# Optimization experiments

Hardware: AMD Instinct MI355X
Metric: run time of the kernel (lower is better)

The kernel has to match this reference:

```python
import jax, jax.numpy as jnp
import numpy as np

NUM_HEADS = 4   # forced by reshape(B, N, num_heads, C) of a dim*4 projection
BN_EPS = 1e-5


def _chamfer(a, b):
    # a, b: [B, N, 3] -> symmetric chamfer distance (mean of nearest sq-dists)
    d = (jnp.sum(a ** 2, -1)[:, :, None] + jnp.sum(b ** 2, -1)[:, None, :]
         - 2.0 * jnp.einsum('bnc,bmc->bnm', a, b))
    return jnp.mean(jnp.min(d, axis=2)) + jnp.mean(jnp.min(d, axis=1))


def _forward(xs, pc1, bn_gamma, bn_beta, q_w, kv_w, proj_w, proj_b, map_w, map_b):
    B, F, C, N = xs.shape
    H = NUM_HEADS
    scale = C ** -0.5  # head_dim == dim in this module (full-dim heads)

    def per_item(x):  # x: [F, C, N]
        # BatchNorm1d in eval mode (running_mean=0, running_var=1)
        xn = (x / jnp.sqrt(1.0 + BN_EPS)) * bn_gamma[:, None] + bn_beta[:, None]
        xn = xn.transpose(0, 2, 1)                 # [F, N, C]
        xr = xn[::-1]                              # flip over frame axis
        q = (xn @ q_w.T).reshape(F, N, H, C).transpose(0, 2, 1, 3)        # [F,H,N,C]
        kv = (xr @ kv_w.T).reshape(F, N, 2, H, C).transpose(2, 0, 3, 1, 4)
        k, v = kv[0], kv[1]                        # [F,H,N,C]
        attn = jax.nn.softmax(jnp.einsum('fhnc,fhmc->fhnm', q, k) * scale, axis=-1)
        o = jnp.einsum('fhnm,fhmc->fhnc', attn, v).transpose(0, 2, 1, 3)  # [F,N,H,C]
        xa = (o[0] + o[1]).transpose(1, 0, 2)      # [H, N, C]: sum of first two frames
        xa = xa @ proj_w.T + proj_b                # [H, N, C] x_appearance
        fr = xa @ map_w.T + map_b                  # [H, N, 3] frames (mapping_xyz)
        return xa, fr

    xa, frames = jax.vmap(per_item)(xs)            # [B,H,N,C], [B,H,N,3]
    pc1t = pc1.transpose(0, 2, 1)                  # [B, N, 3]
    loss = _chamfer(pc1t + frames[:, 0], pc1t)
    return xa[:, 1:], frames[:, 1:], loss


def setup_inputs() -> dict:
    key = jax.random.key(0)
    ks = jax.random.split(key, 8)
    B, F, C, N = 2, 4, 64, 2048
    return {
        'xs': jax.random.normal(ks[0], (B, F, C, N), jnp.float32),
        'pc1': jax.random.normal(ks[1], (B, 3, N), jnp.float32),
        'pc2': jax.random.normal(ks[2], (B, 3, N), jnp.float32),
        'bn_gamma': jnp.ones((C,), jnp.float32),
        'bn_beta': jnp.zeros((C,), jnp.float32),
        'q_w': 0.02 * jax.random.normal(ks[3], (4 * C, C), jnp.float32),
        'kv_w': 0.02 * jax.random.normal(ks[4], (8 * C, C), jnp.float32),
        'proj_w': 0.02 * jax.random.normal(ks[5], (C, C), jnp.float32),
        'proj_b': jnp.zeros((C,), jnp.float32),
        'map_w': 0.02 * jax.random.normal(ks[6], (3, C), jnp.float32),
        'map_b': jnp.zeros((3,), jnp.float32),
    }


def reference(xs, pc1, pc2, bn_gamma, bn_beta, q_w, kv_w, proj_w, proj_b, map_w, map_b):
    # pc2 is accepted by the torch forward but unused in its body
    return _forward(xs, pc1, bn_gamma, bn_beta, q_w, kv_w, proj_w, proj_b, map_w, map_b)
```

## Files before the change

kernel.cpp:

```cpp
#include <hip/hip_runtime.h>
#include <hip/hip_bf16.h>

#define NPTS 2048
#define LOG2E 1.4426950408889634f
#define NJC 16
#define JCH 128

typedef short bf16x8 __attribute__((ext_vector_type(8)));
typedef float f32x4 __attribute__((ext_vector_type(4)));
typedef unsigned uint32x4 __attribute__((ext_vector_type(4)));
typedef __attribute__((address_space(3))) char lds_char;
typedef __attribute__((address_space(1))) const char glob_char;

union PBU { uint32x4 u; bf16x8 v; };

static __device__ __forceinline__ unsigned cvt_pk_bf16(float a, float b) {
    unsigned r;
    asm("v_cvt_pk_bf16_f32 %0, %1, %2" : "=v"(r) : "v"(a), "v"(b));
    return r;
}
static __device__ __forceinline__ float b2f(unsigned short u) {
    return __uint_as_float((unsigned)u << 16);
}

__global__ void prep_weights(const float* __restrict__ gamma, const float* __restrict__ beta,
                             const float* __restrict__ q_w, const float* __restrict__ kv_w,
                             float* __restrict__ Wp, float* __restrict__ bp) {
    int j = blockIdx.x * blockDim.x + threadIdx.x;
    if (j >= 768) return;
    const float inv = 1.0f / sqrtf(1.0f + 1e-5f);
    const float* src;
    float scale;
    if (j < 256) { src = q_w + j * 64;          scale = 0.125f * LOG2E; }
    else         { src = kv_w + (j - 256) * 64; scale = 1.0f; }
    float b = 0.f;
    for (int c = 0; c < 64; ++c) {
        float w = src[c];
        Wp[j * 64 + c] = w * gamma[c] * inv * scale;
        b += w * beta[c];
    }
    bp[j] = b * scale;
}

__global__ __launch_bounds__(256) void qkv_gemm(const float* __restrict__ xs,
                                                const float* __restrict__ Wp,
                                                const float* __restrict__ bp,
                                                __hip_bfloat16* __restrict__ Qg,
                                                __hip_bfloat16* __restrict__ Kg,
                                                __hip_bfloat16* __restrict__ Vtg) {
    const int bf = blockIdx.z;
    const int b = bf >> 1, f01 = bf & 1;
    const int jt = blockIdx.y;
    const int f_src = (jt < 4) ? f01 : (3 - f01);
    const int n0 = blockIdx.x * 64;
    const float* __restrict__ A = xs + (size_t)((b * 4 + f_src) * 64) * NPTS;

    __shared__ float As[64][68];
    __shared__ float Ws[64][68];

    const int t = threadIdx.x;
    const int tx = t & 15, ty = t >> 4;

    for (int r = 0; r < 4; ++r) {
        int row = ty + 16 * r;
        int col = tx * 4;
        *(float4*)&As[row][col] = *(const float4*)&A[(size_t)row * NPTS + n0 + col];
        *(float4*)&Ws[row][col] = *(const float4*)&Wp[(size_t)(jt * 64 + row) * 64 + col];
    }
    __syncthreads();

    float acc[4][4];
#pragma unroll
    for (int jj = 0; jj < 4; ++jj) {
        float bv = bp[jt * 64 + tx + 16 * jj];
#pragma unroll
        for (int i = 0; i < 4; ++i) acc[i][jj] = bv;
    }
    for (int c = 0; c < 64; ++c) {
        float a[4], w[4];
#pragma unroll
        for (int i = 0; i < 4; ++i) a[i] = As[c][ty + 16 * i];
#pragma unroll
        for (int jj = 0; jj < 4; ++jj) w[jj] = Ws[tx + 16 * jj][c];
#pragma unroll
        for (int i = 0; i < 4; ++i)
#pragma unroll
            for (int jj = 0; jj < 4; ++jj) acc[i][jj] += a[i] * w[jj];
    }

    if (jt < 8) {
        __hip_bfloat16* __restrict__ dst = (jt < 4 ? Qg : Kg) + (size_t)bf * NPTS * 256;
        const int jb = (jt & 3) * 64;
#pragma unroll
        for (int i = 0; i < 4; ++i) {
            int n = n0 + ty + 16 * i;
#pragma unroll
            for (int jj = 0; jj < 4; ++jj)
                dst[(size_t)n * 256 + jb + tx + 16 * jj] = __float2bfloat16(acc[i][jj]);
        }
    } else {
        __syncthreads();
#pragma unroll
        for (int i = 0; i < 4; ++i)
#pragma unroll
            for (int jj = 0; jj < 4; ++jj)
                As[tx + 16 * jj][ty + 16 * i] = acc[i][jj];
        __syncthreads();
        const int row = t >> 2, c0 = (t & 3) * 16;
        __hip_bfloat16* __restrict__ dst =
            Vtg + ((size_t)bf * 256 + (jt - 8) * 64 + row) * NPTS + n0 + c0;
#pragma unroll
        for (int c = 0; c < 16; ++c) dst[c] = __float2bfloat16(As[row][c0 + c]);
    }
}

__global__ __launch_bounds__(256, 4) void attn_mfma(const __hip_bfloat16* __restrict__ Qg,
                                                    const __hip_bfloat16* __restrict__ Kg,
                                                    const __hip_bfloat16* __restrict__ Vtg,
                                                    __hip_bfloat16* __restrict__ OTb,
                                                    float* __restrict__ Lp) {
    const int combo = blockIdx.x;
    const int bf = combo >> 2, h = combo & 3;
    const int n0 = blockIdx.y * 128;
    const int split = blockIdx.z;
    const int kbase = split * (NPTS / 4);
    const int NT = NPTS / 4 / 64;

    __shared__ __align__(16) char smem[32768];

    const int t = threadIdx.x;
    const int lane = t & 63, w = t >> 6;
    const int l15 = lane & 15, g = lane >> 4;
    const int srow = lane >> 3, sslot = lane & 7;

    const __hip_bfloat16* qbase =
        Qg + ((size_t)bf * NPTS + n0 + w * 32 + l15) * 256 + h * 64 + g * 8;
    bf16x8 qf[2][2];
    qf[0][0] = *(const bf16x8*)(qbase);
    qf[0][1] = *(const bf16x8*)(qbase + 32);
    qf[1][0] = *(const bf16x8*)(qbase + 16 * 256);
    qf[1][1] = *(const bf16x8*)(qbase + 16 * 256 + 32);

    const __hip_bfloat16* kgb = Kg + (size_t)bf * NPTS * 256 + h * 64;
    const __hip_bfloat16* vgb = Vtg + ((size_t)bf * 256 + h * 64) * NPTS;

    int ldsoff[4][2];
#pragma unroll
    for (int tt = 0; tt < 4; ++tt) {
        const int row = tt * 16 + l15;
#pragma unroll
        for (int s = 0; s < 2; ++s)
            ldsoff[tt][s] = row * 128 + (((s * 4 + g) ^ (row & 7)) << 4);
    }

    f32x4 oacc[2][4];
    float lsum0 = 0.f, lsum1 = 0.f;
#pragma unroll
    for (int f = 0; f < 2; ++f)
#pragma unroll
        for (int r = 0; r < 4; ++r) oacc[f][r] = (f32x4){0.f, 0.f, 0.f, 0.f};

    auto stage = [&](int kt, int bsel) {
#pragma unroll
        for (int ii = 0; ii < 2; ++ii) {
            const int rb = w * 16 + ii * 8;
            const int r = rb + srow;
            const int cs = (sslot ^ (r & 7)) * 8;
            const __hip_bfloat16* ksrc = kgb + (size_t)(kbase + kt * 64 + r) * 256 + cs;
            __builtin_amdgcn_global_load_lds((const glob_char*)ksrc,
                (lds_char*)(smem + bsel * 16384 + rb * 128), 16, 0, 0);
            const __hip_bfloat16* vsrc = vgb + (size_t)r * NPTS + kbase + kt * 64 + cs;
            __builtin_amdgcn_global_load_lds((const glob_char*)vsrc,
                (lds_char*)(smem + bsel * 16384 + 8192 + rb * 128), 16, 0, 0);
        }
    };

    stage(0, 0);
    int cur = 0;

    for (int kt = 0; kt < NT; ++kt) {
        if (kt < NT - 1) {
            stage(kt + 1, cur ^ 1);
            asm volatile("s_waitcnt vmcnt(4)" ::: "memory");
        } else {
            asm volatile("s_waitcnt vmcnt(0)" ::: "memory");
        }
        __builtin_amdgcn_s_barrier();
        asm volatile("" ::: "memory");

        const char* Kt = smem + cur * 16384;
        const char* Vt = Kt + 8192;

        bf16x8 kf[4][2];
#pragma unroll
        for (int tt = 0; tt < 4; ++tt) {
            kf[tt][0] = *(const bf16x8*)(Kt + ldsoff[tt][0]);
            kf[tt][1] = *(const bf16x8*)(Kt + ldsoff[tt][1]);
        }

        bf16x8 pb0[2], pb1[2];

        {
            f32x4 st[4];
            __builtin_amdgcn_s_setprio(1);
#pragma unroll
            for (int tt = 0; tt < 4; ++tt) {
                f32x4 z = (f32x4){0.f, 0.f, 0.f, 0.f};
                z = __builtin_amdgcn_mfma_f32_16x16x32_bf16(kf[tt][0], qf[0][0], z, 0, 0, 0);
                z = __builtin_amdgcn_mfma_f32_16x16x32_bf16(kf[tt][1], qf[0][1], z, 0, 0, 0);
                st[tt] = z;
            }
            __builtin_amdgcn_s_setprio(0);
            unsigned c0[4], c1[4];
#pragma unroll
            for (int tt = 0; tt < 4; ++tt) {
                float p0 = exp2f(fminf(st[tt][0], 126.f));
                float p1 = exp2f(fminf(st[tt][1], 126.f));
                float p2 = exp2f(fminf(st[tt][2], 126.f));
                float p3 = exp2f(fminf(st[tt][3], 126.f));
                lsum0 += (p0 + p1) + (p2 + p3);
                c0[tt] = cvt_pk_bf16(p0, p1);
                c1[tt] = cvt_pk_bf16(p2, p3);
            }
#pragma unroll
            for (int s = 0; s < 2; ++s) {
                unsigned x0 = c0[2 * s], y0 = c0[2 * s + 1];
                unsigned x1 = c1[2 * s], y1 = c1[2 * s + 1];
                asm("v_permlane32_swap_b32 %0, %1" : "+v"(x0), "+v"(y0));
                asm("v_permlane16_swap_b32 %0, %1" : "+v"(x0), "+v"(y0));
                asm("v_permlane32_swap_b32 %0, %1" : "+v"(x1), "+v"(y1));
                asm("v_permlane16_swap_b32 %0, %1" : "+v"(x1), "+v"(y1));
                PBU pu;
                pu.u = (uint32x4){x0, x1, y0, y1};
                pb0[s] = pu.v;
            }
        }

        {
            f32x4 st[4];
            __builtin_amdgcn_s_setprio(1);
#pragma unroll
            for (int tt = 0; tt < 4; ++tt) {
                f32x4 z = (f32x4){0.f, 0.f, 0.f, 0.f};
                z = __builtin_amdgcn_mfma_f32_16x16x32_bf16(kf[tt][0], qf[1][0], z, 0, 0, 0);
                z = __builtin_amdgcn_mfma_f32_16x16x32_bf16(kf[tt][1], qf[1][1], z, 0, 0, 0);
                st[tt] = z;
            }
            __builtin_amdgcn_s_setprio(0);
            unsigned c0[4], c1[4];
#pragma unroll
            for (int tt = 0; tt < 4; ++tt) {
                float p0 = exp2f(fminf(st[tt][0], 126.f));
                float p1 = exp2f(fminf(st[tt][1], 126.f));
                float p2 = exp2f(fminf(st[tt][2], 126.f));
                float p3 = exp2f(fminf(st[tt][3], 126.f));
                lsum1 += (p0 + p1) + (p2 + p3);
                c0[tt] = cvt_pk_bf16(p0, p1);
                c1[tt] = cvt_pk_bf16(p2, p3);
            }
#pragma unroll
            for (int s = 0; s < 2; ++s) {
                unsigned x0 = c0[2 * s], y0 = c0[2 * s + 1];
                unsigned x1 = c1[2 * s], y1 = c1[2 * s + 1];
                asm("v_permlane32_swap_b32 %0, %1" : "+v"(x0), "+v"(y0));
                asm("v_permlane16_swap_b32 %0, %1" : "+v"(x0), "+v"(y0));
                asm("v_permlane32_swap_b32 %0, %1" : "+v"(x1), "+v"(y1));
                asm("v_permlane16_swap_b32 %0, %1" : "+v"(x1), "+v"(y1));
                PBU pu;
                pu.u = (uint32x4){x0, x1, y0, y1};
                pb1[s] = pu.v;
            }
        }

        __builtin_amdgcn_s_setprio(1);
#pragma unroll
        for (int ct = 0; ct < 4; ++ct) {
            bf16x8 vf0 = *(const bf16x8*)(Vt + ldsoff[ct][0]);
            bf16x8 vf1 = *(const bf16x8*)(Vt + ldsoff[ct][1]);
            f32x4 z0 = oacc[0][ct];
            z0 = __builtin_amdgcn_mfma_f32_16x16x32_bf16(vf0, pb0[0], z0, 0, 0, 0);
            z0 = __builtin_amdgcn_mfma_f32_16x16x32_bf16(vf1, pb0[1], z0, 0, 0, 0);
            oacc[0][ct] = z0;
            f32x4 z1 = oacc[1][ct];
            z1 = __builtin_amdgcn_mfma_f32_16x16x32_bf16(vf0, pb1[0], z1, 0, 0, 0);
            z1 = __builtin_amdgcn_mfma_f32_16x16x32_bf16(vf1, pb1[1], z1, 0, 0, 0);
            oacc[1][ct] = z1;
        }
        __builtin_amdgcn_s_setprio(0);

        asm volatile("s_waitcnt lgkmcnt(0)" ::: "memory");
        __builtin_amdgcn_s_barrier();
        asm volatile("" ::: "memory");
        cur ^= 1;
    }

    lsum0 += __shfl_xor(lsum0, 16);
    lsum0 += __shfl_xor(lsum0, 32);
    lsum1 += __shfl_xor(lsum1, 16);
    lsum1 += __shfl_xor(lsum1, 32);
    const int qq = n0 + w * 32 + l15;
    if (g == 0) {
        Lp[(size_t)(split * 16 + combo) * NPTS + qq] = lsum0;
        Lp[(size_t)(split * 16 + combo) * NPTS + qq + 16] = lsum1;
    }

    __hip_bfloat16* __restrict__ Op = OTb + (size_t)(split * 16 + combo) * 64 * NPTS;
#pragma unroll
    for (int ct = 0; ct < 4; ++ct)
#pragma unroll
        for (int r = 0; r < 4; ++r) {
            Op[(size_t)(ct * 16 + g * 4 + r) * NPTS + qq] = __float2bfloat16(oacc[0][ct][r]);
            Op[(size_t)(ct * 16 + g * 4 + r) * NPTS + qq + 16] = __float2bfloat16(oacc[1][ct][r]);
        }
}

__global__ __launch_bounds__(256) void proj_frames(const __hip_bfloat16* __restrict__ OTb,
                                                   const float* __restrict__ Lp,
                                                   const float* __restrict__ proj_w,
                                                   const float* __restrict__ proj_b,
                                                   const float* __restrict__ map_w,
                                                   const float* __restrict__ map_b,
                                                   float* __restrict__ out,
                                                   float* __restrict__ frames0) {
    const int bh = blockIdx.y, b = bh >> 2, h = bh & 3;
    const int n0 = blockIdx.x * 64;
    const int cf0 = (b * 2 + 0) * 4 + h;
    const int cf1 = (b * 2 + 1) * 4 + h;

    __shared__ float Xs[64][68];
    __shared__ float Ws[64][68];
    __shared__ float xaS[64][68];

    const int t = threadIdx.x;
    const int tx = t & 15, ty = t >> 4;
    const int nc = n0 + tx * 4;

    float4 L0 = make_float4(0.f, 0.f, 0.f, 0.f), L1 = L0;
#pragma unroll
    for (int s = 0; s < 4; ++s) {
        float4 a = *(const float4*)&Lp[(size_t)(s * 16 + cf0) * NPTS + nc];
        L0.x += a.x; L0.y += a.y; L0.z += a.z; L0.w += a.w;
        float4 c = *(const float4*)&Lp[(size_t)(s * 16 + cf1) * NPTS + nc];
        L1.x += c.x; L1.y += c.y; L1.z += c.z; L1.w += c.w;
    }
    float4 inv0 = make_float4(1.f / L0.x, 1.f / L0.y, 1.f / L0.z, 1.f / L0.w);
    float4 inv1 = make_float4(1.f / L1.x, 1.f / L1.y, 1.f / L1.z, 1.f / L1.w);

    for (int r = 0; r < 4; ++r) {
        int row = ty + 16 * r, col = tx * 4;
        float x0 = 0.f, x1 = 0.f, x2 = 0.f, x3 = 0.f;
        float y0 = 0.f, y1 = 0.f, y2 = 0.f, y3 = 0.f;
#pragma unroll
        for (int s = 0; s < 4; ++s) {
            ushort4 u0 = *(const ushort4*)&OTb[((size_t)(s * 16 + cf0) * 64 + row) * NPTS + n0 + col];
            ushort4 u1 = *(const ushort4*)&OTb[((size_t)(s * 16 + cf1) * 64 + row) * NPTS + n0 + col];
            x0 += b2f(u0.x); x1 += b2f(u0.y); x2 += b2f(u0.z); x3 += b2f(u0.w);
            y0 += b2f(u1.x); y1 += b2f(u1.y); y2 += b2f(u1.z); y3 += b2f(u1.w);
        }
        Xs[row][col + 0] = x0 * inv0.x + y0 * inv1.x;
        Xs[row][col + 1] = x1 * inv0.y + y1 * inv1.y;
        Xs[row][col + 2] = x2 * inv0.z + y2 * inv1.z;
        Xs[row][col + 3] = x3 * inv0.w + y3 * inv1.w;
        *(float4*)&Ws[row][col] = *(const float4*)&proj_w[(size_t)row * 64 + col];
    }
    __syncthreads();

    float acc[4][4];
#pragma unroll
    for (int jj = 0; jj < 4; ++jj) {
        float bv = proj_b[tx + 16 * jj];
#pragma unroll
        for (int i = 0; i < 4; ++i) acc[i][jj] = bv;
    }
    for (int c = 0; c < 64; ++c) {
        float a[4], w[4];
#pragma unroll
        for (int i = 0; i < 4; ++i) a[i] = Xs[c][ty + 16 * i];
#pragma unroll
        for (int jj = 0; jj < 4; ++jj) w[jj] = Ws[tx + 16 * jj][c];
#pragma unroll
        for (int i = 0; i < 4; ++i)
#pragma unroll
            for (int jj = 0; jj < 4; ++jj) acc[i][jj] += a[i] * w[jj];
    }

#pragma unroll
    for (int i = 0; i < 4; ++i)
#pragma unroll
        for (int jj = 0; jj < 4; ++jj)
            xaS[ty + 16 * i][tx + 16 * jj] = acc[i][jj];

    if (h >= 1) {
        float* __restrict__ xa_out = out + (size_t)(b * 3 + h - 1) * NPTS * 64;
#pragma unroll
        for (int i = 0; i < 4; ++i)
#pragma unroll
            for (int jj = 0; jj < 4; ++jj)
                xa_out[(size_t)(n0 + ty + 16 * i) * 64 + tx + 16 * jj] = acc[i][jj];
    }
    __syncthreads();

    if (t < 192) {
        int r = t / 3, j = t % 3;
        float s = map_b[j];
        for (int c = 0; c < 64; ++c) s += xaS[r][c] * map_w[j * 64 + c];
        int n = n0 + r;
        if (h == 0) frames0[((size_t)b * NPTS + n) * 3 + j] = s;
        else        out[786432 + ((size_t)(b * 3 + h - 1) * NPTS + n) * 3 + j] = s;
    }
}

__global__ __launch_bounds__(256) void chamfer_partial(const float* __restrict__ pc1,
                                                       const float* __restrict__ frames0,
                                                       float* __restrict__ partial) {
    const int z = blockIdx.z;
    const int dir = z >> 1, b = z & 1;
    const int i = blockIdx.x * 256 + threadIdx.x;
    const int j0 = blockIdx.y * JCH;
    const float* __restrict__ px = pc1 + (size_t)b * 3 * NPTS;
    const float* __restrict__ fr = frames0 + (size_t)b * NPTS * 3;

    __shared__ float4 sj[JCH];
    if (threadIdx.x < JCH) {
        int jj = j0 + threadIdx.x;
        float bx = px[jj], by = px[NPTS + jj], bz = px[2 * NPTS + jj];
        if (dir == 1) { bx += fr[jj * 3]; by += fr[jj * 3 + 1]; bz += fr[jj * 3 + 2]; }
        sj[threadIdx.x] = make_float4(bx, by, bz, bx * bx + by * by + bz * bz);
    }
    float ax = px[i], ay = px[NPTS + i], az = px[2 * NPTS + i];
    if (dir == 0) { ax += fr[i * 3]; ay += fr[i * 3 + 1]; az += fr[i * 3 + 2]; }
    const float a2 = ax * ax + ay * ay + az * az;
    __syncthreads();

    float best = 1e30f;
#pragma unroll 4
    for (int k = 0; k < JCH; ++k) {
        float4 p = sj[k];
        float d = a2 + p.w - 2.0f * (ax * p.x + ay * p.y + az * p.z);
        best = fminf(best, d);
    }
    partial[((size_t)z * NJC + blockIdx.y) * NPTS + i] = best;
}

__global__ __launch_bounds__(256) void chamfer_minsum(const float* __restrict__ partial,
                                                      double* __restrict__ sums) {
    const int gid = blockIdx.x * 256 + threadIdx.x;
    const int z = gid >> 11, i = gid & 2047;
    float best = 1e30f;
#pragma unroll
    for (int c = 0; c < NJC; ++c)
        best = fminf(best, partial[((size_t)z * NJC + c) * NPTS + i]);
    __shared__ double sm[256];
    sm[threadIdx.x] = (double)best;
    __syncthreads();
    for (int off = 128; off > 0; off >>= 1) {
        if (threadIdx.x < off) sm[threadIdx.x] += sm[threadIdx.x + off];
        __syncthreads();
    }
    if (threadIdx.x == 0) sums[blockIdx.x] = sm[0];
}

__global__ void chamfer_final(const double* __restrict__ sums, float* __restrict__ loss_out) {
    if (threadIdx.x == 0) {
        double s = 0.0;
        for (int k = 0; k < 32; ++k) s += sums[k];
        loss_out[0] = (float)(s / 4096.0);
    }
}

extern "C" void kernel_launch(void* const* d_in, const int* in_sizes, int n_in,
                              void* d_out, int out_size, void* d_ws, size_t ws_size,
                              hipStream_t stream) {
    const float* xs     = (const float*)d_in[0];
    const float* pc1    = (const float*)d_in[1];
    const float* gamma  = (const float*)d_in[3];
    const float* beta   = (const float*)d_in[4];
    const float* q_w    = (const float*)d_in[5];
    const float* kv_w   = (const float*)d_in[6];
    const float* proj_w = (const float*)d_in[7];
    const float* proj_b = (const float*)d_in[8];
    const float* map_w  = (const float*)d_in[9];
    const float* map_b  = (const float*)d_in[10];
    float* out = (float*)d_out;

    char* ws = (char*)d_ws;
    __hip_bfloat16* Qg  = (__hip_bfloat16*)(ws);
    __hip_bfloat16* Kg  = (__hip_bfloat16*)(ws + 4194304);
    __hip_bfloat16* Vtg = (__hip_bfloat16*)(ws + 8388608);
    __hip_bfloat16* OTb = (__hip_bfloat16*)(ws + 12582912);
    float* Wp      = (float*)(ws + 29360128);
    float* bp      = (float*)(ws + 29556736);
    float* frames0 = (float*)(ws + 29559808);
    float* partial = (float*)(ws + 29609984);
    double* sums   = (double*)(ws + 30134272);
    float* Lp      = (float*)(ws + 30134528);

    hipLaunchKernelGGL(prep_weights, dim3(3), dim3(256), 0, stream,
                       gamma, beta, q_w, kv_w, Wp, bp);
    hipLaunchKernelGGL(qkv_gemm, dim3(32, 12, 4), dim3(256), 0, stream,
                       xs, Wp, bp, Qg, Kg, Vtg);
    hipLaunchKernelGGL(attn_mfma, dim3(16, 16, 4), dim3(256), 0, stream,
                       Qg, Kg, Vtg, OTb, Lp);
    hipLaunchKernelGGL(proj_frames, dim3(32, 8), dim3(256), 0, stream,
                       OTb, Lp, proj_w, proj_b, map_w, map_b, out, frames0);
    hipLaunchKernelGGL(chamfer_partial, dim3(NPTS / 256, NJC, 4), dim3(256), 0, stream,
                       pc1, frames0, partial);
    hipLaunchKernelGGL(chamfer_minsum, dim3(32), dim3(256), 0, stream,
                       partial, sums);
    hipLaunchKernelGGL(chamfer_final, dim3(1), dim3(64), 0, stream,
                       sums, out + 823296);
}
```

Measured before the change: 91.86 us.

## Shrink attention KV tile to 32 rows with 4-slot ring buffer, two-deep prefetch

The attention kernel now processes 32-key tiles instead of 64 and cycles them through a 4-entry LDS ring with two tiles prefetched ahead. That allows one barrier per tile instead of two. The V LDS layout and swizzle change to match the narrower tile. The aim is better overlap of global-to-LDS loads with MFMA work and less barrier stall, at the cost of twice as many loop iterations and barriers per key range. The setprio hints are also dropped.

```diff
diff --git a/kernel.cpp b/kernel.cpp
--- a/kernel.cpp
+++ b/kernel.cpp
@@ -124,14 +124,18 @@
     const int n0 = blockIdx.y * 128;
     const int split = blockIdx.z;
     const int kbase = split * (NPTS / 4);
-    const int NT = NPTS / 4 / 64;
+    const int NT = NPTS / 4 / 32;
 
     __shared__ __align__(16) char smem[32768];
 
     const int t = threadIdx.x;
     const int lane = t & 63, w = t >> 6;
-    const int l15 = lane & 15, g = lane >> 4;
-    const int srow = lane >> 3, sslot = lane & 7;
+    const int l15 = lane & 15, g = (lane >> 4) & 3;
+
+    const int krow = w * 8 + (lane >> 3), kslot = lane & 7;
+    const int vrow = w * 16 + (lane >> 2), vslot = lane & 3;
+    const int kcs = (kslot ^ (krow & 7)) * 8;
+    const int vcs = (vslot ^ ((vrow >> 1) & 3)) * 8;
 
     const __hip_bfloat16* qbase =
         Qg + ((size_t)bf * NPTS + n0 + w * 32 + l15) * 256 + h * 64 + g * 8;
@@ -144,164 +148,114 @@
     const __hip_bfloat16* kgb = Kg + (size_t)bf * NPTS * 256 + h * 64;
     const __hip_bfloat16* vgb = Vtg + ((size_t)bf * 256 + h * 64) * NPTS;
 
-    int ldsoff[4][2];
-#pragma unroll
-    for (int tt = 0; tt < 4; ++tt) {
+    int koff[2][2], voff[4];
+#pragma unroll
+    for (int tt = 0; tt < 2; ++tt) {
         const int row = tt * 16 + l15;
 #pragma unroll
         for (int s = 0; s < 2; ++s)
-            ldsoff[tt][s] = row * 128 + (((s * 4 + g) ^ (row & 7)) << 4);
+            koff[tt][s] = row * 128 + (((s * 4 + g) ^ (row & 7)) << 4);
+    }
+#pragma unroll
+    for (int ct = 0; ct < 4; ++ct) {
+        const int row = ct * 16 + l15;
+        voff[ct] = 4096 + row * 64 + ((g ^ ((row >> 1) & 3)) << 4);
     }
 
     f32x4 oacc[2][4];
-    float lsum0 = 0.f, lsum1 = 0.f;
+    float lsum[2] = {0.f, 0.f};
 #pragma unroll
     for (int f = 0; f < 2; ++f)
 #pragma unroll
         for (int r = 0; r < 4; ++r) oacc[f][r] = (f32x4){0.f, 0.f, 0.f, 0.f};
 
-    auto stage = [&](int kt, int bsel) {
-#pragma unroll
-        for (int ii = 0; ii < 2; ++ii) {
-            const int rb = w * 16 + ii * 8;
-            const int r = rb + srow;
-            const int cs = (sslot ^ (r & 7)) * 8;
-            const __hip_bfloat16* ksrc = kgb + (size_t)(kbase + kt * 64 + r) * 256 + cs;
-            __builtin_amdgcn_global_load_lds((const glob_char*)ksrc,
-                (lds_char*)(smem + bsel * 16384 + rb * 128), 16, 0, 0);
-            const __hip_bfloat16* vsrc = vgb + (size_t)r * NPTS + kbase + kt * 64 + cs;
-            __builtin_amdgcn_global_load_lds((const glob_char*)vsrc,
-                (lds_char*)(smem + bsel * 16384 + 8192 + rb * 128), 16, 0, 0);
+    auto stage = [&](int kt) {
+        const int bsel = kt & 3;
+        const __hip_bfloat16* ksrc = kgb + (size_t)(kbase + kt * 32 + krow) * 256 + kcs;
+        __builtin_amdgcn_global_load_lds((const glob_char*)ksrc,
+            (lds_char*)(smem + bsel * 8192 + w * 1024), 16, 0, 0);
+        const __hip_bfloat16* vsrc = vgb + (size_t)vrow * NPTS + kbase + kt * 32 + vcs;
+        __builtin_amdgcn_global_load_lds((const glob_char*)vsrc,
+            (lds_char*)(smem + bsel * 8192 + 4096 + w * 1024), 16, 0, 0);
+    };
+
+    auto tile = [&](int kt) {
+        const char* B = smem + (kt & 3) * 8192;
+        bf16x8 kf[2][2];
+#pragma unroll
+        for (int tt = 0; tt < 2; ++tt)
+#pragma unroll
+            for (int s = 0; s < 2; ++s)
+                kf[tt][s] = *(const bf16x8*)(B + koff[tt][s]);
+
+        bf16x8 pb[2];
+#pragma unroll
+        for (int f = 0; f < 2; ++f) {
+            f32x4 st0 = (f32x4){0.f, 0.f, 0.f, 0.f}, st1 = st0;
+            st0 = __builtin_amdgcn_mfma_f32_16x16x32_bf16(kf[0][0], qf[f][0], st0, 0, 0, 0);
+            st0 = __builtin_amdgcn_mfma_f32_16x16x32_bf16(kf[0][1], qf[f][1], st0, 0, 0, 0);
+            st1 = __builtin_amdgcn_mfma_f32_16x16x32_bf16(kf[1][0], qf[f][0], st1, 0, 0, 0);
+            st1 = __builtin_amdgcn_mfma_f32_16x16x32_bf16(kf[1][1], qf[f][1], st1, 0, 0, 0);
+            float p00 = exp2f(fminf(st0[0], 126.f));
+            float p01 = exp2f(fminf(st0[1], 126.f));
+            float p02 = exp2f(fminf(st0[2], 126.f));
+            float p03 = exp2f(fminf(st0[3], 126.f));
+            float p10 = exp2f(fminf(st1[0], 126.f));
+            float p11 = exp2f(fminf(st1[1], 126.f));
+            float p12 = exp2f(fminf(st1[2], 126.f));
+            float p13 = exp2f(fminf(st1[3], 126.f));
+            lsum[f] += ((p00 + p01) + (p02 + p03)) + ((p10 + p11) + (p12 + p13));
+            unsigned x0 = cvt_pk_bf16(p00, p01);
+            unsigned x1 = cvt_pk_bf16(p02, p03);
+            unsigned y0 = cvt_pk_bf16(p10, p11);
+            unsigned y1 = cvt_pk_bf16(p12, p13);
+            asm("v_permlane32_swap_b32 %0, %1" : "+v"(x0), "+v"(y0));
+            asm("v_permlane16_swap_b32 %0, %1" : "+v"(x0), "+v"(y0));
+            asm("v_permlane32_swap_b32 %0, %1" : "+v"(x1), "+v"(y1));
+            asm("v_permlane16_swap_b32 %0, %1" : "+v"(x1), "+v"(y1));
+            PBU pu;
+            pu.u = (uint32x4){x0, x1, y0, y1};
+            pb[f] = pu.v;
+        }
+
+#pragma unroll
+        for (int ct = 0; ct < 4; ++ct) {
+            bf16x8 vf = *(const bf16x8*)(B + voff[ct]);
+            oacc[0][ct] = __builtin_amdgcn_mfma_f32_16x16x32_bf16(vf, pb[0], oacc[0][ct], 0, 0, 0);
+            oacc[1][ct] = __builtin_amdgcn_mfma_f32_16x16x32_bf16(vf, pb[1], oacc[1][ct], 0, 0, 0);
         }
     };
 
-    stage(0, 0);
-    int cur = 0;
-
-    for (int kt = 0; kt < NT; ++kt) {
-        if (kt < NT - 1) {
-            stage(kt + 1, cur ^ 1);
-            asm volatile("s_waitcnt vmcnt(4)" ::: "memory");
-        } else {
-            asm volatile("s_waitcnt vmcnt(0)" ::: "memory");
-        }
-        __builtin_amdgcn_s_barrier();
-        asm volatile("" ::: "memory");
-
-        const char* Kt = smem + cur * 16384;
-        const char* Vt = Kt + 8192;
-
-        bf16x8 kf[4][2];
-#pragma unroll
-        for (int tt = 0; tt < 4; ++tt) {
-            kf[tt][0] = *(const bf16x8*)(Kt + ldsoff[tt][0]);
-            kf[tt][1] = *(const bf16x8*)(Kt + ldsoff[tt][1]);
-        }
-
-        bf16x8 pb0[2], pb1[2];
-
-        {
-            f32x4 st[4];
-            __builtin_amdgcn_s_setprio(1);
-#pragma unroll
-            for (int tt = 0; tt < 4; ++tt) {
-                f32x4 z = (f32x4){0.f, 0.f, 0.f, 0.f};
-                z = __builtin_amdgcn_mfma_f32_16x16x32_bf16(kf[tt][0], qf[0][0], z, 0, 0, 0);
-                z = __builtin_amdgcn_mfma_f32_16x16x32_bf16(kf[tt][1], qf[0][1], z, 0, 0, 0);
-                st[tt] = z;
-            }
-            __builtin_amdgcn_s_setprio(0);
-            unsigned c0[4], c1[4];
-#pragma unroll
-            for (int tt = 0; tt < 4; ++tt) {
-                float p0 = exp2f(fminf(st[tt][0], 126.f));
-                float p1 = exp2f(fminf(st[tt][1], 126.f));
-                float p2 = exp2f(fminf(st[tt][2], 126.f));
-                float p3 = exp2f(fminf(st[tt][3], 126.f));
-                lsum0 += (p0 + p1) + (p2 + p3);
-                c0[tt] = cvt_pk_bf16(p0, p1);
-                c1[tt] = cvt_pk_bf16(p2, p3);
-            }
-#pragma unroll
-            for (int s = 0; s < 2; ++s) {
-                unsigned x0 = c0[2 * s], y0 = c0[2 * s + 1];
-                unsigned x1 = c1[2 * s], y1 = c1[2 * s + 1];
-                asm("v_permlane32_swap_b32 %0, %1" : "+v"(x0), "+v"(y0));
-                asm("v_permlane16_swap_b32 %0, %1" : "+v"(x0), "+v"(y0));
-                asm("v_permlane32_swap_b32 %0, %1" : "+v"(x1), "+v"(y1));
-                asm("v_permlane16_swap_b32 %0, %1" : "+v"(x1), "+v"(y1));
-                PBU pu;
-                pu.u = (uint32x4){x0, x1, y0, y1};
-                pb0[s] = pu.v;
-            }
-        }
-
-        {
-            f32x4 st[4];
-            __builtin_amdgcn_s_setprio(1);
-#pragma unroll
-            for (int tt = 0; tt < 4; ++tt) {
-                f32x4 z = (f32x4){0.f, 0.f, 0.f, 0.f};
-                z = __builtin_amdgcn_mfma_f32_16x16x32_bf16(kf[tt][0], qf[1][0], z, 0, 0, 0);
-                z = __builtin_amdgcn_mfma_f32_16x16x32_bf16(kf[tt][1], qf[1][1], z, 0, 0, 0);
-                st[tt] = z;
-            }
-            __builtin_amdgcn_s_setprio(0);
-            unsigned c0[4], c1[4];
-#pragma unroll
-            for (int tt = 0; tt < 4; ++tt) {
-                float p0 = exp2f(fminf(st[tt][0], 126.f));
-                float p1 = exp2f(fminf(st[tt][1], 126.f));
-                float p2 = exp2f(fminf(st[tt][2], 126.f));
-                float p3 = exp2f(fminf(st[tt][3], 126.f));
-                lsum1 += (p0 + p1) + (p2 + p3);
-                c0[tt] = cvt_pk_bf16(p0, p1);
-                c1[tt] = cvt_pk_bf16(p2, p3);
-            }
-#pragma unroll
-            for (int s = 0; s < 2; ++s) {
-                unsigned x0 = c0[2 * s], y0 = c0[2 * s + 1];
-                unsigned x1 = c1[2 * s], y1 = c1[2 * s + 1];
-                asm("v_permlane32_swap_b32 %0, %1" : "+v"(x0), "+v"(y0));
-                asm("v_permlane16_swap_b32 %0, %1" : "+v"(x0), "+v"(y0));
-                asm("v_permlane32_swap_b32 %0, %1" : "+v"(x1), "+v"(y1));
-                asm("v_permlane16_swap_b32 %0, %1" : "+v"(x1), "+v"(y1));
-                PBU pu;
-                pu.u = (uint32x4){x0, x1, y0, y1};
-                pb1[s] = pu.v;
-            }
-        }
-
-        __builtin_amdgcn_s_setprio(1);
-#pragma unroll
-        for (int ct = 0; ct < 4; ++ct) {
-            bf16x8 vf0 = *(const bf16x8*)(Vt + ldsoff[ct][0]);
-            bf16x8 vf1 = *(const bf16x8*)(Vt + ldsoff[ct][1]);
-            f32x4 z0 = oacc[0][ct];
-            z0 = __builtin_amdgcn_mfma_f32_16x16x32_bf16(vf0, pb0[0], z0, 0, 0, 0);
-            z0 = __builtin_amdgcn_mfma_f32_16x16x32_bf16(vf1, pb0[1], z0, 0, 0, 0);
-            oacc[0][ct] = z0;
-            f32x4 z1 = oacc[1][ct];
-            z1 = __builtin_amdgcn_mfma_f32_16x16x32_bf16(vf0, pb1[0], z1, 0, 0, 0);
-            z1 = __builtin_amdgcn_mfma_f32_16x16x32_bf16(vf1, pb1[1], z1, 0, 0, 0);
-            oacc[1][ct] = z1;
-        }
-        __builtin_amdgcn_s_setprio(0);
-
+    stage(0);
+    stage(1);
+    for (int kt = 0; kt < NT - 2; ++kt) {
+        stage(kt + 2);
+        asm volatile("s_waitcnt vmcnt(4)" ::: "memory");
         asm volatile("s_waitcnt lgkmcnt(0)" ::: "memory");
         __builtin_amdgcn_s_barrier();
         asm volatile("" ::: "memory");
-        cur ^= 1;
-    }
-
-    lsum0 += __shfl_xor(lsum0, 16);
-    lsum0 += __shfl_xor(lsum0, 32);
-    lsum1 += __shfl_xor(lsum1, 16);
-    lsum1 += __shfl_xor(lsum1, 32);
+        tile(kt);
+    }
+    asm volatile("s_waitcnt vmcnt(2)" ::: "memory");
+    asm volatile("s_waitcnt lgkmcnt(0)" ::: "memory");
+    __builtin_amdgcn_s_barrier();
+    asm volatile("" ::: "memory");
+    tile(NT - 2);
+    asm volatile("s_waitcnt vmcnt(0)" ::: "memory");
+    asm volatile("s_waitcnt lgkmcnt(0)" ::: "memory");
+    __builtin_amdgcn_s_barrier();
+    asm volatile("" ::: "memory");
+    tile(NT - 1);
+
+    float l0 = lsum[0], l1 = lsum[1];
+    l0 += __shfl_xor(l0, 16);
+    l0 += __shfl_xor(l0, 32);
+    l1 += __shfl_xor(l1, 16);
+    l1 += __shfl_xor(l1, 32);
     const int qq = n0 + w * 32 + l15;
     if (g == 0) {
-        Lp[(size_t)(split * 16 + combo) * NPTS + qq] = lsum0;
-        Lp[(size_t)(split * 16 + combo) * NPTS + qq + 16] = lsum1;
+        Lp[(size_t)(split * 16 + combo) * NPTS + qq] = l0;
+        Lp[(size_t)(split * 16 + combo) * NPTS + qq + 16] = l1;
     }
 
     __hip_bfloat16* __restrict__ Op = OTb + (size_t)(split * 16 + combo) * 64 * NPTS;
```

New measurement: 89.25 us. -2.8%, faster.
